# Performance work log

Hardware: AMD Instinct MI355X
Metric: run time of the kernel (lower is better)

## Reference

```python
import jax, jax.numpy as jnp
import numpy as np

N = 65536   # nodes
D = 128     # in_dim == emb_dim (required by GRUCell usage)
E = 524288  # edges, pre-sorted by topological level
L = 8       # number of topological levels (edge_masks)


def _gru(x, h, Wi, Wh, bi, bh):
    # torch.nn.GRUCell semantics
    gi = x @ Wi.T + bi            # [*, 3D]
    gh = h @ Wh.T + bh
    ir, iz, i_n = jnp.split(gi, 3, axis=-1)
    hr, hz, h_n = jnp.split(gh, 3, axis=-1)
    r = jax.nn.sigmoid(ir + hr)
    z = jax.nn.sigmoid(iz + hz)
    n = jnp.tanh(i_n + r * h_n)
    return (1.0 - z) * n + z * h


def _direction(h_prev, j_lev, i_lev, ea_lev, We, be, Wa, ba, Wi, Wh, bi, bh):
    # j = message source (h_j gathered), i = aggregation target (segment index)
    n_nodes = h_prev.shape[0]
    # roots = nodes never appearing as aggregation target -> GRU with zero hidden
    root = ~jnp.zeros((n_nodes,), bool).at[i_lev.reshape(-1)].set(True)
    h = jnp.where(root[:, None], _gru(h_prev, jnp.zeros_like(h_prev), Wi, Wh, bi, bh), 0.0)

    def step(h, lev):
        j, i, ea = lev                       # [El], [El], [El, D]
        e = ea @ We.T + be                   # edge_lin
        q = h_prev[i]                        # h_prev_i
        k = h[j] + e                         # h_j + edge_emb
        v = h[j]
        alpha = (jnp.concatenate([q, k], axis=-1) @ Wa.T + ba)[:, 0]  # [El]
        # segment softmax over aggregation index i (numerically stable)
        m = jax.lax.stop_gradient(jax.ops.segment_max(alpha, i, num_segments=n_nodes))
        ex = jnp.exp(alpha - m[i])
        den = jax.ops.segment_sum(ex, i, num_segments=n_nodes)
        a = ex / den[i]
        msg = jax.ops.segment_sum(a[:, None] * v, i, num_segments=n_nodes)  # [N, D]
        mask = jnp.zeros((n_nodes,), bool).at[i].set(True)
        h_new = _gru(h_prev, msg, Wi, Wh, bi, bh)
        return jnp.where(mask[:, None], h_new, h), None

    h, _ = jax.lax.scan(step, h, (j_lev, i_lev, ea_lev))
    return h


def setup_inputs() -> dict:
    key = jax.random.key(0)
    ks = jax.random.split(key, 24)
    p = lambda k, shape: (0.05 * jax.random.normal(k, shape)).astype(jnp.float32)
    inp = {
        'x': jax.random.normal(ks[0], (N, D), jnp.float32),
        'edge_index': jax.random.randint(ks[1], (2, E), 0, N, dtype=jnp.int32),
        'edge_attr': jax.random.normal(ks[2], (E, D), jnp.float32),
        'num_levels': L,
        # forward-direction AttnConv + GRUCell params
        'We_f': p(ks[3], (D, D)), 'be_f': p(ks[4], (D,)),
        'Wa_f': p(ks[5], (1, 2 * D)), 'ba_f': p(ks[6], (1,)),
        'Wi_f': p(ks[7], (3 * D, D)), 'Wh_f': p(ks[8], (3 * D, D)),
        'bi_f': p(ks[9], (3 * D,)), 'bh_f': p(ks[10], (3 * D,)),
        # backward-direction params
        'We_b': p(ks[11], (D, D)), 'be_b': p(ks[12], (D,)),
        'Wa_b': p(ks[13], (1, 2 * D)), 'ba_b': p(ks[14], (1,)),
        'Wi_b': p(ks[15], (3 * D, D)), 'Wh_b': p(ks[16], (3 * D, D)),
        'bi_b': p(ks[17], (3 * D,)), 'bh_b': p(ks[18], (3 * D,)),
    }
    return inp


def reference(x, edge_index, edge_attr, num_levels,
              We_f, be_f, Wa_f, ba_f, Wi_f, Wh_f, bi_f, bh_f,
              We_b, be_b, Wa_b, ba_b, Wi_b, Wh_b, bi_b, bh_b):
    El = edge_index.shape[1] // num_levels
    src = edge_index[0].reshape(num_levels, El)
    dst = edge_index[1].reshape(num_levels, El)
    ea = edge_attr.reshape(num_levels, El, -1)
    # forward pass over levels: flow source->target, aggregate at dst
    h_fwd = _direction(x, src, dst, ea, We_f, be_f, Wa_f, ba_f, Wi_f, Wh_f, bi_f, bh_f)
    # fnb: backward pass takes h_fwd as h_prev; flow target->source (aggregate at src),
    # levels iterated in reverse
    h_bwd = _direction(h_fwd, dst[::-1], src[::-1], ea[::-1],
                       We_b, be_b, Wa_b, ba_b, Wi_b, Wh_b, bi_b, bh_b)
    return jax.nn.relu(h_bwd)
```

## Files before the change

kernel.cpp:

```cpp
#include <hip/hip_runtime.h>
#include <cstdint>
#include <cstddef>

constexpr int N_NODES = 65536;
constexpr int D       = 128;
constexpr int E_EDGES = 524288;
constexpr int LVLS    = 8;
constexpr int EL      = E_EDGES / LVLS;
constexpr int OSTR    = 65540;

typedef unsigned int  u32;
typedef unsigned short u16;
typedef __attribute__((ext_vector_type(8)))  short short8;
typedef __attribute__((ext_vector_type(16))) float f32x16;

__device__ __forceinline__ float sigmoidf_(float x) { return 1.0f / (1.0f + expf(-x)); }

__device__ __forceinline__ u32 bf_hi(float f) {
    u32 x = __float_as_uint(f);
    return (x + 0x7fffu + ((x >> 16) & 1u)) >> 16;
}
__device__ __forceinline__ float bf_f(u32 hbits) { return __uint_as_float(hbits << 16); }

__device__ __forceinline__ int swz(int row, int kbyte) {
    return row * 64 + (kbyte ^ ((row & 3) << 4));
}

__device__ __forceinline__ void gload_lds16(const void* g, void* l) {
    __builtin_amdgcn_global_load_lds(
        (const __attribute__((address_space(1))) unsigned int*)g,
        (__attribute__((address_space(3))) unsigned int*)l, 16, 0, 0);
}

__device__ __forceinline__ float wave_sum(float v) {
#pragma unroll
    for (int off = 32; off > 0; off >>= 1) v += __shfl_down(v, off, 64);
    return v;
}

__global__ __launch_bounds__(256)
void prep_kernel(const float* __restrict__ We_f, const float* __restrict__ Wa_f,
                 const float* __restrict__ be_f, const float* __restrict__ ba_f,
                 const float* __restrict__ We_b, const float* __restrict__ Wa_b,
                 const float* __restrict__ be_b, const float* __restrict__ ba_b,
                 float* __restrict__ u_f, float* __restrict__ u_b, float* __restrict__ cst)
{
    int t = threadIdx.x;
    if (t < 128) {
        float s = 0.f;
        for (int d = 0; d < 128; ++d) s = fmaf(We_f[d * 128 + t], Wa_f[128 + d], s);
        u_f[t] = s;
    } else {
        int c = t - 128;
        float s = 0.f;
        for (int d = 0; d < 128; ++d) s = fmaf(We_b[d * 128 + c], Wa_b[128 + d], s);
        u_b[c] = s;
    }
    if (t == 0) {
        float s = 0.f;
        for (int d = 0; d < 128; ++d) s = fmaf(be_f[d], Wa_f[128 + d], s);
        cst[0] = s + ba_f[0];
    }
    if (t == 255) {
        float s = 0.f;
        for (int d = 0; d < 128; ++d) s = fmaf(be_b[d], Wa_b[128 + d], s);
        cst[1] = s + ba_b[0];
    }
}

__global__ __launch_bounds__(256)
void convert_w(const float* __restrict__ W0, const float* __restrict__ W1,
               const float* __restrict__ W2, const float* __restrict__ W3,
               u16* __restrict__ hi4, u16* __restrict__ lo4)
{
    const float* Ws[4] = {W0, W1, W2, W3};
    int m = blockIdx.y;
    int i = blockIdx.x * 256 + threadIdx.x;
    int rw = i >> 7, k = i & 127;
    float v = Ws[m][i];
    u32 hb = bf_hi(v);
    hi4[(size_t)m * 49152 + i] = (u16)hb;
    if (rw >= 256)
        lo4[(size_t)m * 16384 + (size_t)(rw - 256) * 128 + k] = (u16)bf_hi(v - bf_f(hb));
}

__global__ __launch_bounds__(256)
void convert_x(const float* __restrict__ x, unsigned char* __restrict__ xhi,
               unsigned char* __restrict__ xlo)
{
    int idx = blockIdx.x * 256 + threadIdx.x;
    int n = idx >> 6, d = (idx & 63) << 1;
    float2 v = *reinterpret_cast<const float2*>(x + (size_t)n * 128 + d);
    u32 h0 = bf_hi(v.x), h1 = bf_hi(v.y);
    u32 l0 = bf_hi(v.x - bf_f(h0)), l1 = bf_hi(v.y - bf_f(h1));
    size_t off = (size_t)n * 256 + (size_t)d * 2;
    *reinterpret_cast<u32*>(xhi + off) = h0 | (h1 << 16);
    *reinterpret_cast<u32*>(xlo + off) = l0 | (l1 << 16);
}

__global__ __launch_bounds__(256)
void edot_count(const float* __restrict__ ea, const float* __restrict__ u_f,
                const float* __restrict__ u_b, const float* __restrict__ cst,
                const int* __restrict__ ei,
                float* __restrict__ edot_f, float* __restrict__ edot_b,
                int* __restrict__ counts, int* __restrict__ flag_f,
                int* __restrict__ flag_b)
{
    int wv = threadIdx.x >> 6, lane = threadIdx.x & 63;
    int e = blockIdx.x * 4 + wv;
    if (e >= E_EDGES) return;
    int d = lane << 1;
    float2 v  = *reinterpret_cast<const float2*>(ea + (size_t)e * 128 + d);
    float2 uf = *reinterpret_cast<const float2*>(u_f + d);
    float2 ub = *reinterpret_cast<const float2*>(u_b + d);
    float af = wave_sum(v.x * uf.x + v.y * uf.y);
    float ab = wave_sum(v.x * ub.x + v.y * ub.y);
    if (lane == 0) {
        edot_f[e] = af + cst[0];
        edot_b[e] = ab + cst[1];
        int lv = e >> 16;
        int s = ei[e], t = ei[E_EDGES + e];
        atomicAdd(&counts[(size_t)lv * 65536 + t], 1);
        atomicAdd(&counts[(size_t)(8 + lv) * 65536 + s], 1);
        flag_f[t] = 1;
        flag_b[s] = 1;
    }
}

__global__ __launch_bounds__(1024)
void scan_compact(const int* __restrict__ counts, int* __restrict__ offs,
                  int* __restrict__ rows, int* __restrict__ cnts)
{
    __shared__ int sbuf[1024];
    __shared__ int nbuf[1024];
    int dl = blockIdx.x;
    const int4* c4 = reinterpret_cast<const int4*>(counts + (size_t)dl * 65536);
    int* o = offs + (size_t)dl * OSTR;
    int* rw = rows + (size_t)dl * 65536;
    int t = threadIdx.x;
    int cv[64];
#pragma unroll 4
    for (int k4 = 0; k4 < 16; ++k4) {
        int4 v = c4[t * 16 + k4];
        cv[k4 * 4 + 0] = v.x; cv[k4 * 4 + 1] = v.y;
        cv[k4 * 4 + 2] = v.z; cv[k4 * 4 + 3] = v.w;
    }
    int s = 0, nz = 0;
#pragma unroll
    for (int k = 0; k < 64; ++k) { s += cv[k]; nz += (cv[k] > 0); }
    sbuf[t] = s;
    nbuf[t] = nz;
    __syncthreads();
    int val = s, nval = nz;
    for (int off = 1; off < 1024; off <<= 1) {
        int add  = (t >= off) ? sbuf[t - off] : 0;
        int nadd = (t >= off) ? nbuf[t - off] : 0;
        __syncthreads();
        val += add;
        nval += nadd;
        sbuf[t] = val;
        nbuf[t] = nval;
        __syncthreads();
    }
    int run  = val - s;
    int nrun = nval - nz;
    int base = t * 64;
    int4* o4 = reinterpret_cast<int4*>(o + base);
#pragma unroll 4
    for (int k4 = 0; k4 < 16; ++k4) {
        int4 ov;
        ov.x = run; run += cv[k4 * 4 + 0];
        ov.y = run; run += cv[k4 * 4 + 1];
        ov.z = run; run += cv[k4 * 4 + 2];
        ov.w = run; run += cv[k4 * 4 + 3];
        o4[k4] = ov;
#pragma unroll
        for (int q = 0; q < 4; ++q)
            if (cv[k4 * 4 + q] > 0) rw[nrun++] = base + k4 * 4 + q;
    }
    if (t == 1023) { o[65536] = val; cnts[dl] = nval; }
}

__global__ __launch_bounds__(256)
void fill_csr(const int* __restrict__ ei, const float* __restrict__ edot_f,
              const float* __restrict__ edot_b, const int* __restrict__ offs,
              int* __restrict__ cursor, int2* __restrict__ csr)
{
    int idx = blockIdx.x * 256 + threadIdx.x;
    int dir = idx >= E_EDGES;
    int ge = dir ? idx - E_EDGES : idx;
    int lv = ge >> 16;
    int dl = dir * 8 + lv;
    int i = dir ? ei[ge] : ei[E_EDGES + ge];
    int j = dir ? ei[E_EDGES + ge] : ei[ge];
    int pos = offs[(size_t)dl * OSTR + i] + atomicAdd(&cursor[(size_t)dl * 65536 + i], 1);
    int2 v;
    v.x = j;
    v.y = __float_as_int(dir ? edot_b[ge] : edot_f[ge]);
    csr[(size_t)dl * EL + pos] = v;
}

__global__ __launch_bounds__(256)
void root_init(const float* __restrict__ hp, const int* __restrict__ flag,
               const float* __restrict__ Wi, const float* __restrict__ bi,
               const float* __restrict__ bh, const float* __restrict__ wa,
               float* __restrict__ h, unsigned char* __restrict__ h_hi,
               unsigned char* __restrict__ h_lo, int write_img,
               float* __restrict__ qdot, float* __restrict__ hdot)
{
    int wv = threadIdx.x >> 6, lane = threadIdx.x & 63;
    int n = blockIdx.x * 4 + wv;
    int d = lane << 1;
    const float* hprow = hp + (size_t)n * 128;
    float2 hpv = *reinterpret_cast<const float2*>(hprow + d);
    float qd = wave_sum(hpv.x * wa[d] + hpv.y * wa[d + 1]);
    if (lane == 0) qdot[n] = qd;
    bool root = (flag[n] == 0);
    float hv[2] = {0.f, 0.f};
    if (root) {
#pragma unroll
        for (int q = 0; q < 2; ++q) {
            int dd = d + q;
            float g0 = bi[dd], g1 = bi[dd + 128], g2 = bi[dd + 256];
            for (int k = 0; k < 128; ++k) {
                float a = hprow[k];
                g0 = fmaf(a, Wi[(size_t)dd * 128 + k], g0);
                g1 = fmaf(a, Wi[(size_t)(dd + 128) * 128 + k], g1);
                g2 = fmaf(a, Wi[(size_t)(dd + 256) * 128 + k], g2);
            }
            float rr = sigmoidf_(g0 + bh[dd]);
            float zz = sigmoidf_(g1 + bh[dd + 128]);
            float nn = tanhf(g2 + rr * bh[dd + 256]);
            hv[q] = (1.f - zz) * nn;
        }
        *reinterpret_cast<float2*>(h + (size_t)n * 128 + d) = make_float2(hv[0], hv[1]);
        if (write_img) {
            u32 hb0 = bf_hi(hv[0]), hb1 = bf_hi(hv[1]);
            u32 lb0 = bf_hi(hv[0] - bf_f(hb0)), lb1 = bf_hi(hv[1] - bf_f(hb1));
            size_t off = (size_t)n * 256 + (size_t)d * 2;
            *reinterpret_cast<u32*>(h_hi + off) = hb0 | (hb1 << 16);
            *reinterpret_cast<u32*>(h_lo + off) = lb0 | (lb1 << 16);
        }
    }
    float hd = wave_sum(hv[0] * wa[128 + d] + hv[1] * wa[128 + d + 1]);
    if (lane == 0) hdot[n] = root ? hd : 0.f;
}

__global__ __launch_bounds__(256)
void attn_msg(const int* __restrict__ pcnt, const int* __restrict__ rows,
              const int* __restrict__ offs, const int2* __restrict__ csr,
              const float* __restrict__ qdot, const float* __restrict__ hdot,
              const float* __restrict__ h, unsigned char* __restrict__ msg_hi)
{
    int cnt = *pcnt;
    int l31 = threadIdx.x & 31;
    int hid = (blockIdx.x * 256 + threadIdx.x) >> 5;
    int nh = (gridDim.x * 256) >> 5;
    int d4 = l31 << 2;
    for (int r = hid; r < cnt; r += nh) {
        int i = rows[r];
        int o0 = offs[i], o1 = offs[i + 1];
        float qi = qdot[i];
        float den = 0.f;
        float4 acc = make_float4(0.f, 0.f, 0.f, 0.f);
        int2 je = csr[o0];
        for (int e = o0; e < o1; ++e) {
            int en = e + 1;
            int2 jn = (en < o1) ? csr[en] : je;
            float ex = expf(qi + hdot[je.x] + __int_as_float(je.y));
            float4 hv = *reinterpret_cast<const float4*>(h + (size_t)je.x * 128 + d4);
            den += ex;
            acc.x = fmaf(ex, hv.x, acc.x);
            acc.y = fmaf(ex, hv.y, acc.y);
            acc.z = fmaf(ex, hv.z, acc.z);
            acc.w = fmaf(ex, hv.w, acc.w);
            je = jn;
        }
        float inv = 1.f / den;
        u32 h0 = bf_hi(acc.x * inv), h1 = bf_hi(acc.y * inv);
        u32 h2 = bf_hi(acc.z * inv), h3 = bf_hi(acc.w * inv);
        *reinterpret_cast<uint2*>(msg_hi + (size_t)r * 256 + (size_t)d4 * 2) =
            make_uint2(h0 | (h1 << 16), h2 | (h3 << 16));
    }
}

__global__ __launch_bounds__(256, 2)
void gemm_gru(const unsigned char* __restrict__ msg_hi,
              const unsigned char* __restrict__ hp_hi, const unsigned char* __restrict__ hp_lo,
              const u16* __restrict__ Whhi,
              const u16* __restrict__ Wihi, const u16* __restrict__ Wilo,
              const int* __restrict__ pcnt, const int* __restrict__ rows,
              const float* __restrict__ bi, const float* __restrict__ bh,
              const float* __restrict__ wa,
              float* __restrict__ h, unsigned char* __restrict__ h_hi,
              unsigned char* __restrict__ h_lo, int write_img,
              float* __restrict__ hdot)
{
    __shared__ __align__(16) unsigned char smem[16384 + 65536];
    unsigned char* As = smem;
    unsigned char* Bs = smem + 16384;

    const int tid = threadIdx.x;
    const int cnt = *pcnt;
    const int row0 = blockIdx.x * 64;
    if (row0 >= cnt) return;

    const int lane = tid & 63, wv = tid >> 6;
    const int q = wv;
    const int l31 = lane & 31, l5 = lane >> 5;

    const int rwA = wv * 16 + (lane >> 2);
    const int slA = ((lane & 3) << 4) ^ ((rwA & 3) << 4);
    int garA = row0 + rwA;
    const size_t baseA0 = (size_t)garA * 256 + slA;
    int rowA1 = rows[garA < cnt ? garA : 0];
    const size_t baseA1 = (size_t)rowA1 * 256 + slA;
    size_t bsrc[6];
#pragma unroll
    for (int k = 0; k < 6; ++k) {
        int rwB = wv * 96 + k * 16 + (lane >> 2);
        bsrc[k] = (size_t)rwB * 256 + (((lane & 3) << 4) ^ ((rwB & 3) << 4));
    }
    size_t lsrc[2];
#pragma unroll
    for (int k = 0; k < 2; ++k) {
        int rwL = wv * 32 + k * 16 + (lane >> 2);
        lsrc[k] = (size_t)rwL * 256 + (((lane & 3) << 4) ^ ((rwL & 3) << 4));
    }

    f32x16 acc[2][3];
#pragma unroll
    for (int mt = 0; mt < 2; ++mt)
#pragma unroll
        for (int g = 0; g < 3; ++g) acc[mt][g] = (f32x16)0.0f;
    f32x16 ghn[2];

    auto STAGE = [&](int tt) {
        int b = tt & 1;
        size_t ko = (size_t)(tt & 3) * 64;
        unsigned char* Bd = Bs + b * 32768;
        if (tt < 4) {
            gload_lds16(msg_hi + baseA0 + ko, As + b * 8192 + wv * 1024);
#pragma unroll
            for (int k = 0; k < 6; ++k)
                gload_lds16((const unsigned char*)Whhi + bsrc[k] + ko, Bd + (wv * 6 + k) * 1024);
        } else {
            gload_lds16(hp_hi + baseA1 + ko, As + b * 8192 + wv * 1024);
            gload_lds16(hp_lo + baseA1 + ko, As + b * 8192 + 4096 + wv * 1024);
#pragma unroll
            for (int k = 0; k < 6; ++k)
                gload_lds16((const unsigned char*)Wihi + bsrc[k] + ko, Bd + (wv * 6 + k) * 1024);
#pragma unroll
            for (int k = 0; k < 2; ++k)
                gload_lds16((const unsigned char*)Wilo + lsrc[k] + ko, Bd + 24576 + (wv * 2 + k) * 1024);
        }
    };

    STAGE(0);
    for (int t = 0; t < 8; ++t) {
        if (t < 7) STAGE(t + 1);
        __builtin_amdgcn_sched_barrier(0);
        if (t < 3)      asm volatile("s_waitcnt vmcnt(7)");
        else if (t < 7) asm volatile("s_waitcnt vmcnt(10)");
        else            asm volatile("s_waitcnt vmcnt(0)");
        __builtin_amdgcn_s_barrier();
        __builtin_amdgcn_sched_barrier(0);

        const unsigned char* Ab = As + (t & 1) * 8192;
        const unsigned char* Bb = Bs + (t & 1) * 32768;
#pragma unroll
        for (int kh = 0; kh < 2; ++kh) {
            short8 b0 = *reinterpret_cast<const short8*>(
                Bb + swz(q * 32 + l31, kh * 32 + l5 * 16));
            short8 b1 = *reinterpret_cast<const short8*>(
                Bb + swz(q * 32 + 128 + l31, kh * 32 + l5 * 16));
            short8 b2 = *reinterpret_cast<const short8*>(
                Bb + swz(q * 32 + 256 + l31, kh * 32 + l5 * 16));
            short8 ah[2];
#pragma unroll
            for (int mt = 0; mt < 2; ++mt)
                ah[mt] = *reinterpret_cast<const short8*>(
                    Ab + swz(mt * 32 + l31, kh * 32 + l5 * 16));
            if (t < 4) {
#pragma unroll
                for (int mt = 0; mt < 2; ++mt) {
                    acc[mt][0] = __builtin_amdgcn_mfma_f32_32x32x16_bf16(ah[mt], b0, acc[mt][0], 0, 0, 0);
                    acc[mt][1] = __builtin_amdgcn_mfma_f32_32x32x16_bf16(ah[mt], b1, acc[mt][1], 0, 0, 0);
                    acc[mt][2] = __builtin_amdgcn_mfma_f32_32x32x16_bf16(ah[mt], b2, acc[mt][2], 0, 0, 0);
                }
            } else {
                short8 bl2 = *reinterpret_cast<const short8*>(
                    Bb + 24576 + swz(q * 32 + l31, kh * 32 + l5 * 16));
                short8 al[2];
#pragma unroll
                for (int mt = 0; mt < 2; ++mt)
                    al[mt] = *reinterpret_cast<const short8*>(
                        Ab + 4096 + swz(mt * 32 + l31, kh * 32 + l5 * 16));
#pragma unroll
                for (int mt = 0; mt < 2; ++mt) {
                    acc[mt][0] = __builtin_amdgcn_mfma_f32_32x32x16_bf16(ah[mt], b0, acc[mt][0], 0, 0, 0);
                    acc[mt][0] = __builtin_amdgcn_mfma_f32_32x32x16_bf16(al[mt], b0, acc[mt][0], 0, 0, 0);
                    acc[mt][1] = __builtin_amdgcn_mfma_f32_32x32x16_bf16(ah[mt], b1, acc[mt][1], 0, 0, 0);
                    acc[mt][1] = __builtin_amdgcn_mfma_f32_32x32x16_bf16(al[mt], b1, acc[mt][1], 0, 0, 0);
                    acc[mt][2] = __builtin_amdgcn_mfma_f32_32x32x16_bf16(ah[mt], b2, acc[mt][2], 0, 0, 0);
                    acc[mt][2] = __builtin_amdgcn_mfma_f32_32x32x16_bf16(ah[mt], bl2, acc[mt][2], 0, 0, 0);
                    acc[mt][2] = __builtin_amdgcn_mfma_f32_32x32x16_bf16(al[mt], b2, acc[mt][2], 0, 0, 0);
                }
            }
        }
        if (t == 3) {
            ghn[0] = acc[0][2];
            ghn[1] = acc[1][2];
            acc[0][2] = (f32x16)0.0f;
            acc[1][2] = (f32x16)0.0f;
        }
        __builtin_amdgcn_s_barrier();
        __builtin_amdgcn_sched_barrier(0);
    }

    __syncthreads();
    float* red = (float*)Bs;
    const int d = q * 32 + l31;
    const float wa2d = wa[128 + d];
    const float bi0 = bi[d], bi1 = bi[d + 128], bi2 = bi[d + 256];
    const float bh0 = bh[d], bh1 = bh[d + 128], bh2 = bh[d + 256];

#pragma unroll
    for (int mt = 0; mt < 2; ++mt)
#pragma unroll
        for (int rg = 0; rg < 16; ++rg) {
            int rl = mt * 32 + (rg & 3) + ((rg >> 2) << 3) + (l5 << 2);
            int gr = row0 + rl;
            bool ok = gr < cnt;
            int n = rows[ok ? gr : 0];
            float mval = bf_f(*reinterpret_cast<const u16*>(
                msg_hi + (size_t)gr * 256 + (size_t)d * 2));
            float rr = sigmoidf_(acc[mt][0][rg] + bi0 + bh0);
            float zz = sigmoidf_(acc[mt][1][rg] + bi1 + bh1);
            float nn = tanhf(acc[mt][2][rg] + bi2 + rr * (ghn[mt][rg] + bh2));
            float hv = (1.f - zz) * nn + zz * mval;
            if (ok) {
                h[(size_t)n * 128 + d] = hv;
                if (write_img) {
                    u32 hb = bf_hi(hv);
                    *reinterpret_cast<u16*>(h_hi + (size_t)n * 256 + (size_t)d * 2) = (u16)hb;
                    *reinterpret_cast<u16*>(h_lo + (size_t)n * 256 + (size_t)d * 2) =
                        (u16)bf_hi(hv - bf_f(hb));
                }
            }
            float pd = hv * wa2d;
#pragma unroll
            for (int o = 1; o < 32; o <<= 1) pd += __shfl_xor(pd, o, 64);
            if (l31 == 0) red[rl * 4 + q] = pd;
        }
    __syncthreads();
    if (tid < 64 && row0 + tid < cnt) {
        int n = rows[row0 + tid];
        hdot[n] = red[tid * 4] + red[tid * 4 + 1] + red[tid * 4 + 2] + red[tid * 4 + 3];
    }
}

__global__ __launch_bounds__(256)
void relu_kernel(const float* __restrict__ h, float* __restrict__ out)
{
    int idx = (blockIdx.x * 256 + threadIdx.x) * 4;
    float4 v = *reinterpret_cast<const float4*>(h + idx);
    v.x = fmaxf(v.x, 0.f); v.y = fmaxf(v.y, 0.f);
    v.z = fmaxf(v.z, 0.f); v.w = fmaxf(v.w, 0.f);
    *reinterpret_cast<float4*>(out + idx) = v;
}

extern "C" void kernel_launch(void* const* d_in, const int* in_sizes, int n_in,
                              void* d_out, int out_size, void* d_ws, size_t ws_size,
                              hipStream_t stream)
{
    (void)in_sizes; (void)n_in; (void)out_size; (void)ws_size;

    const float* x    = (const float*)d_in[0];
    const int*   ei   = (const int*)d_in[1];
    const float* ea   = (const float*)d_in[2];
    const float* We_f = (const float*)d_in[4];
    const float* be_f = (const float*)d_in[5];
    const float* Wa_f = (const float*)d_in[6];
    const float* ba_f = (const float*)d_in[7];
    const float* Wi_f = (const float*)d_in[8];
    const float* Wh_f = (const float*)d_in[9];
    const float* bi_f = (const float*)d_in[10];
    const float* bh_f = (const float*)d_in[11];
    const float* We_b = (const float*)d_in[12];
    const float* be_b = (const float*)d_in[13];
    const float* Wa_b = (const float*)d_in[14];
    const float* ba_b = (const float*)d_in[15];
    const float* Wi_b = (const float*)d_in[16];
    const float* Wh_b = (const float*)d_in[17];
    const float* bi_b = (const float*)d_in[18];
    const float* bh_b = (const float*)d_in[19];
    float* out = (float*)d_out;

    char* p = (char*)d_ws;
    auto carve = [&](size_t bytes) -> char* {
        char* r = p;
        p += (bytes + 255) & ~(size_t)255;
        return r;
    };
    int*   counts  = (int*)carve((size_t)16 * 65536 * 4);
    int*   cursor  = (int*)carve((size_t)16 * 65536 * 4);
    int*   flag_f  = (int*)carve((size_t)N_NODES * 4);
    int*   flag_b  = (int*)carve((size_t)N_NODES * 4);
    float* h_fwd   = (float*)carve((size_t)N_NODES * D * 4);
    float* h_cur   = (float*)carve((size_t)N_NODES * D * 4);
    size_t zbytes  = (size_t)((char*)h_cur - (char*)counts) + (size_t)N_NODES * D * 4;
    unsigned char* hf_hi = (unsigned char*)carve((size_t)N_NODES * 256);
    unsigned char* hf_lo = (unsigned char*)carve((size_t)N_NODES * 256);
    int*   cnts    = (int*)carve(256);
    u16*   Whi4    = (u16*)carve((size_t)4 * 49152 * 2);
    u16*   Wlo4    = (u16*)carve((size_t)4 * 16384 * 2);
    unsigned char* x_hi  = (unsigned char*)carve((size_t)N_NODES * 256);
    unsigned char* x_lo  = (unsigned char*)carve((size_t)N_NODES * 256);
    unsigned char* msg_hi= (unsigned char*)carve((size_t)N_NODES * 256);
    float* u_f     = (float*)carve((size_t)D * 4);
    float* u_b     = (float*)carve((size_t)D * 4);
    float* cst     = (float*)carve(16);
    float* edot_f  = (float*)carve((size_t)E_EDGES * 4);
    float* edot_b  = (float*)carve((size_t)E_EDGES * 4);
    int*   offs    = (int*)carve((size_t)16 * OSTR * 4);
    int2*  csr     = (int2*)carve((size_t)16 * EL * 8);
    int*   rows    = (int*)carve((size_t)16 * 65536 * 4);
    float* qdot    = (float*)carve((size_t)N_NODES * 4);
    float* hdot    = (float*)carve((size_t)N_NODES * 4);

    hipMemsetAsync(counts, 0, zbytes, stream);
    prep_kernel<<<1, 256, 0, stream>>>(We_f, Wa_f, be_f, ba_f, We_b, Wa_b, be_b, ba_b,
                                       u_f, u_b, cst);
    convert_w<<<dim3(192, 4), 256, 0, stream>>>(Wi_f, Wh_f, Wi_b, Wh_b, Whi4, Wlo4);
    convert_x<<<16384, 256, 0, stream>>>(x, x_hi, x_lo);
    edot_count<<<E_EDGES / 4, 256, 0, stream>>>(ea, u_f, u_b, cst, ei,
                                                edot_f, edot_b, counts, flag_f, flag_b);
    scan_compact<<<16, 1024, 0, stream>>>(counts, offs, rows, cnts);
    fill_csr<<<2 * E_EDGES / 256, 256, 0, stream>>>(ei, edot_f, edot_b, offs, cursor, csr);

    for (int dir = 0; dir < 2; ++dir) {
        const float* hp   = dir == 0 ? x : h_fwd;
        float*       h    = dir == 0 ? h_fwd : h_cur;
        const unsigned char* hp_hi = dir == 0 ? x_hi : hf_hi;
        const unsigned char* hp_lo = dir == 0 ? x_lo : hf_lo;
        unsigned char* h_hi = hf_hi;
        unsigned char* h_lo = hf_lo;
        int write_img = (dir == 0);
        const u16* Wihi = Whi4 + (size_t)(dir * 2) * 49152;
        const u16* Whhi = Whi4 + (size_t)(dir * 2 + 1) * 49152;
        const u16* Wilo = Wlo4 + (size_t)(dir * 2) * 16384;
        const float* Wi   = dir == 0 ? Wi_f : Wi_b;
        const float* bi   = dir == 0 ? bi_f : bi_b;
        const float* bh   = dir == 0 ? bh_f : bh_b;
        const float* wa   = dir == 0 ? Wa_f : Wa_b;
        const int*   flag = dir == 0 ? flag_f : flag_b;

        root_init<<<N_NODES / 4, 256, 0, stream>>>(hp, flag, Wi, bi, bh, wa,
                                                   h, h_hi, h_lo, write_img, qdot, hdot);

        for (int t = 0; t < LVLS; ++t) {
            int lv = dir == 0 ? t : (LVLS - 1 - t);
            int dl = dir * LVLS + lv;
            attn_msg<<<2048, 256, 0, stream>>>(
                cnts + dl, rows + (size_t)dl * 65536, offs + (size_t)dl * OSTR,
                csr + (size_t)dl * EL, qdot, hdot, h, msg_hi);
            gemm_gru<<<1024, 256, 0, stream>>>(
                msg_hi, hp_hi, hp_lo, Whhi, Wihi, Wilo,
                cnts + dl, rows + (size_t)dl * 65536,
                bi, bh, wa, h, h_hi, h_lo, write_img, hdot);
        }
    }
    relu_kernel<<<(N_NODES * D) / 1024, 256, 0, stream>>>(h_cur, out);
}
```

Before: 1.480 ms.

## Gather bf16 hidden image in attention and batch edge dot products per wave

The attention aggregation now gathers neighbour hidden states from a bf16 image (half the bytes of fp32) instead of the fp32 h buffer. To support this, the backward direction also writes a bf16 hi image into a new zero-initialised buffer, while the lo image stays forward-only. Separately, edot_count now has each wave process 8 edges with interleaved shuffle reductions, splitting the forward and backward atomics across lanes. The bf16 gather lowers the precision of message accumulation, and the memset region grows to cover the new buffer.

```diff
diff --git a/kernel.cpp b/kernel.cpp
--- a/kernel.cpp
+++ b/kernel.cpp
@@ -107,23 +107,44 @@
                 int* __restrict__ flag_b)
 {
     int wv = threadIdx.x >> 6, lane = threadIdx.x & 63;
-    int e = blockIdx.x * 4 + wv;
-    if (e >= E_EDGES) return;
+    int e0 = (blockIdx.x * 4 + wv) * 8;
     int d = lane << 1;
-    float2 v  = *reinterpret_cast<const float2*>(ea + (size_t)e * 128 + d);
     float2 uf = *reinterpret_cast<const float2*>(u_f + d);
     float2 ub = *reinterpret_cast<const float2*>(u_b + d);
-    float af = wave_sum(v.x * uf.x + v.y * uf.y);
-    float ab = wave_sum(v.x * ub.x + v.y * ub.y);
-    if (lane == 0) {
-        edot_f[e] = af + cst[0];
-        edot_b[e] = ab + cst[1];
+    float af[8], ab[8];
+#pragma unroll
+    for (int k = 0; k < 8; ++k) {
+        float2 v = *reinterpret_cast<const float2*>(ea + (size_t)(e0 + k) * 128 + d);
+        af[k] = v.x * uf.x + v.y * uf.y;
+        ab[k] = v.x * ub.x + v.y * ub.y;
+    }
+#pragma unroll
+    for (int off = 1; off < 64; off <<= 1) {
+#pragma unroll
+        for (int k = 0; k < 8; ++k) {
+            af[k] += __shfl_xor(af[k], off, 64);
+            ab[k] += __shfl_xor(ab[k], off, 64);
+        }
+    }
+    if (lane < 16) {
+        int k = lane & 7;
+        int e = e0 + k;
         int lv = e >> 16;
-        int s = ei[e], t = ei[E_EDGES + e];
-        atomicAdd(&counts[(size_t)lv * 65536 + t], 1);
-        atomicAdd(&counts[(size_t)(8 + lv) * 65536 + s], 1);
-        flag_f[t] = 1;
-        flag_b[s] = 1;
+        float sf = k == 0 ? af[0] : k == 1 ? af[1] : k == 2 ? af[2] : k == 3 ? af[3] :
+                   k == 4 ? af[4] : k == 5 ? af[5] : k == 6 ? af[6] : af[7];
+        float sb = k == 0 ? ab[0] : k == 1 ? ab[1] : k == 2 ? ab[2] : k == 3 ? ab[3] :
+                   k == 4 ? ab[4] : k == 5 ? ab[5] : k == 6 ? ab[6] : ab[7];
+        if (lane < 8) {
+            edot_f[e] = sf + cst[0];
+            int t = ei[E_EDGES + e];
+            atomicAdd(&counts[(size_t)lv * 65536 + t], 1);
+            flag_f[t] = 1;
+        } else {
+            edot_b[e] = sb + cst[1];
+            int s = ei[e];
+            atomicAdd(&counts[(size_t)(8 + lv) * 65536 + s], 1);
+            flag_b[s] = 1;
+        }
     }
 }
 
@@ -205,7 +226,7 @@
                const float* __restrict__ Wi, const float* __restrict__ bi,
                const float* __restrict__ bh, const float* __restrict__ wa,
                float* __restrict__ h, unsigned char* __restrict__ h_hi,
-               unsigned char* __restrict__ h_lo, int write_img,
+               unsigned char* __restrict__ h_lo, int write_lo,
                float* __restrict__ qdot, float* __restrict__ hdot)
 {
     int wv = threadIdx.x >> 6, lane = threadIdx.x & 63;
@@ -234,11 +255,11 @@
             hv[q] = (1.f - zz) * nn;
         }
         *reinterpret_cast<float2*>(h + (size_t)n * 128 + d) = make_float2(hv[0], hv[1]);
-        if (write_img) {
-            u32 hb0 = bf_hi(hv[0]), hb1 = bf_hi(hv[1]);
+        u32 hb0 = bf_hi(hv[0]), hb1 = bf_hi(hv[1]);
+        size_t off = (size_t)n * 256 + (size_t)d * 2;
+        *reinterpret_cast<u32*>(h_hi + off) = hb0 | (hb1 << 16);
+        if (write_lo) {
             u32 lb0 = bf_hi(hv[0] - bf_f(hb0)), lb1 = bf_hi(hv[1] - bf_f(hb1));
-            size_t off = (size_t)n * 256 + (size_t)d * 2;
-            *reinterpret_cast<u32*>(h_hi + off) = hb0 | (hb1 << 16);
             *reinterpret_cast<u32*>(h_lo + off) = lb0 | (lb1 << 16);
         }
     }
@@ -250,7 +271,7 @@
 void attn_msg(const int* __restrict__ pcnt, const int* __restrict__ rows,
               const int* __restrict__ offs, const int2* __restrict__ csr,
               const float* __restrict__ qdot, const float* __restrict__ hdot,
-              const float* __restrict__ h, unsigned char* __restrict__ msg_hi)
+              const unsigned char* __restrict__ h_img, unsigned char* __restrict__ msg_hi)
 {
     int cnt = *pcnt;
     int l31 = threadIdx.x & 31;
@@ -268,12 +289,17 @@
             int en = e + 1;
             int2 jn = (en < o1) ? csr[en] : je;
             float ex = expf(qi + hdot[je.x] + __int_as_float(je.y));
-            float4 hv = *reinterpret_cast<const float4*>(h + (size_t)je.x * 128 + d4);
+            uint2 w = *reinterpret_cast<const uint2*>(
+                h_img + (size_t)je.x * 256 + (size_t)d4 * 2);
+            float v0 = __uint_as_float(w.x << 16);
+            float v1 = __uint_as_float(w.x & 0xffff0000u);
+            float v2 = __uint_as_float(w.y << 16);
+            float v3 = __uint_as_float(w.y & 0xffff0000u);
             den += ex;
-            acc.x = fmaf(ex, hv.x, acc.x);
-            acc.y = fmaf(ex, hv.y, acc.y);
-            acc.z = fmaf(ex, hv.z, acc.z);
-            acc.w = fmaf(ex, hv.w, acc.w);
+            acc.x = fmaf(ex, v0, acc.x);
+            acc.y = fmaf(ex, v1, acc.y);
+            acc.z = fmaf(ex, v2, acc.z);
+            acc.w = fmaf(ex, v3, acc.w);
             je = jn;
         }
         float inv = 1.f / den;
@@ -293,7 +319,7 @@
               const float* __restrict__ bi, const float* __restrict__ bh,
               const float* __restrict__ wa,
               float* __restrict__ h, unsigned char* __restrict__ h_hi,
-              unsigned char* __restrict__ h_lo, int write_img,
+              unsigned char* __restrict__ h_lo, int write_lo,
               float* __restrict__ hdot)
 {
     __shared__ __align__(16) unsigned char smem[16384 + 65536];
@@ -441,12 +467,11 @@
             float hv = (1.f - zz) * nn + zz * mval;
             if (ok) {
                 h[(size_t)n * 128 + d] = hv;
-                if (write_img) {
-                    u32 hb = bf_hi(hv);
-                    *reinterpret_cast<u16*>(h_hi + (size_t)n * 256 + (size_t)d * 2) = (u16)hb;
+                u32 hb = bf_hi(hv);
+                *reinterpret_cast<u16*>(h_hi + (size_t)n * 256 + (size_t)d * 2) = (u16)hb;
+                if (write_lo)
                     *reinterpret_cast<u16*>(h_lo + (size_t)n * 256 + (size_t)d * 2) =
                         (u16)bf_hi(hv - bf_f(hb));
-                }
             }
             float pd = hv * wa2d;
 #pragma unroll
@@ -509,8 +534,9 @@
     int*   flag_b  = (int*)carve((size_t)N_NODES * 4);
     float* h_fwd   = (float*)carve((size_t)N_NODES * D * 4);
     float* h_cur   = (float*)carve((size_t)N_NODES * D * 4);
-    size_t zbytes  = (size_t)((char*)h_cur - (char*)counts) + (size_t)N_NODES * D * 4;
     unsigned char* hf_hi = (unsigned char*)carve((size_t)N_NODES * 256);
+    unsigned char* hc_hi = (unsigned char*)carve((size_t)N_NODES * 256);
+    size_t zbytes  = (size_t)((char*)hc_hi - (char*)counts) + (size_t)N_NODES * 256;
     unsigned char* hf_lo = (unsigned char*)carve((size_t)N_NODES * 256);
     int*   cnts    = (int*)carve(256);
     u16*   Whi4    = (u16*)carve((size_t)4 * 49152 * 2);
@@ -534,8 +560,8 @@
                                        u_f, u_b, cst);
     convert_w<<<dim3(192, 4), 256, 0, stream>>>(Wi_f, Wh_f, Wi_b, Wh_b, Whi4, Wlo4);
     convert_x<<<16384, 256, 0, stream>>>(x, x_hi, x_lo);
-    edot_count<<<E_EDGES / 4, 256, 0, stream>>>(ea, u_f, u_b, cst, ei,
-                                                edot_f, edot_b, counts, flag_f, flag_b);
+    edot_count<<<E_EDGES / 32, 256, 0, stream>>>(ea, u_f, u_b, cst, ei,
+                                                 edot_f, edot_b, counts, flag_f, flag_b);
     scan_compact<<<16, 1024, 0, stream>>>(counts, offs, rows, cnts);
     fill_csr<<<2 * E_EDGES / 256, 256, 0, stream>>>(ei, edot_f, edot_b, offs, cursor, csr);
 
@@ -544,9 +570,9 @@
         float*       h    = dir == 0 ? h_fwd : h_cur;
         const unsigned char* hp_hi = dir == 0 ? x_hi : hf_hi;
         const unsigned char* hp_lo = dir == 0 ? x_lo : hf_lo;
-        unsigned char* h_hi = hf_hi;
+        unsigned char* h_hi = dir == 0 ? hf_hi : hc_hi;
         unsigned char* h_lo = hf_lo;
-        int write_img = (dir == 0);
+        int write_lo = (dir == 0);
         const u16* Wihi = Whi4 + (size_t)(dir * 2) * 49152;
         const u16* Whhi = Whi4 + (size_t)(dir * 2 + 1) * 49152;
         const u16* Wilo = Wlo4 + (size_t)(dir * 2) * 16384;
@@ -557,18 +583,18 @@
         const int*   flag = dir == 0 ? flag_f : flag_b;
 
         root_init<<<N_NODES / 4, 256, 0, stream>>>(hp, flag, Wi, bi, bh, wa,
-                                                   h, h_hi, h_lo, write_img, qdot, hdot);
+                                                   h, h_hi, h_lo, write_lo, qdot, hdot);
 
         for (int t = 0; t < LVLS; ++t) {
             int lv = dir == 0 ? t : (LVLS - 1 - t);
             int dl = dir * LVLS + lv;
             attn_msg<<<2048, 256, 0, stream>>>(
                 cnts + dl, rows + (size_t)dl * 65536, offs + (size_t)dl * OSTR,
-                csr + (size_t)dl * EL, qdot, hdot, h, msg_hi);
+                csr + (size_t)dl * EL, qdot, hdot, h_hi, msg_hi);
             gemm_gru<<<1024, 256, 0, stream>>>(
                 msg_hi, hp_hi, hp_lo, Whhi, Wihi, Wilo,
                 cnts + dl, rows + (size_t)dl * 65536,
-                bi, bh, wa, h, h_hi, h_lo, write_img, hdot);
+                bi, bh, wa, h, h_hi, h_lo, write_lo, hdot);
         }
     }
     relu_kernel<<<(N_NODES * D) / 1024, 256, 0, stream>>>(h_cur, out);
```

Result: faster. 1.416 ms (-4.3%).
